# Performance work log

Measured on AMD Instinct MI355X. Metric: run time of the kernel, lower is better.

Reference implementation:

```python
import jax, jax.numpy as jnp
import numpy as np

EPS = 1e-12
B, C, H, M, E, P = 2, 20000, 64, 8, 200000, 3


def setup_inputs() -> dict:
    key = jax.random.key(0)
    ks = jax.random.split(key, 24)
    inp = {}
    inp["features"] = jax.random.normal(ks[0], (B, C, H), jnp.float32)
    inp["positions"] = jax.random.normal(ks[1], (B, C, P), jnp.float32)
    inp["edge_index"] = jax.random.randint(ks[2], (2, E), 0, C)
    inp["degree"] = jax.random.randint(ks[3], (C,), 1, 33).astype(jnp.float32)
    inp["cell_node_indices"] = jax.random.randint(ks[4], (C, M), 0, C)
    mask = (jax.random.uniform(ks[5], (C, M)) > 0.3).astype(jnp.float32)
    inp["cell_node_mask"] = mask.at[:, 0].set(1.0)  # first node always valid (pad semantics)

    def lin(k, fan_in, fan_out):
        return (jax.random.normal(k, (fan_in, fan_out), jnp.float32) / np.sqrt(fan_in)).astype(jnp.float32)

    # message MLP: Linear(2H+4 -> H), SiLU, Linear(H -> H)
    inp["W1"] = lin(ks[6], 2 * H + 4, H); inp["b1"] = jnp.zeros((H,), jnp.float32)
    inp["W2"] = lin(ks[7], H, H);         inp["b2"] = jnp.zeros((H,), jnp.float32)
    # position MLP: Linear(H -> H), SiLU, Linear(H -> 1)
    inp["P1"] = lin(ks[8], H, H);  inp["pb1"] = jnp.zeros((H,), jnp.float32)
    inp["P2"] = lin(ks[9], H, 1);  inp["pb2"] = jnp.zeros((1,), jnp.float32)
    # update MLP: Linear(2H -> H), SiLU, Linear(H -> H)
    inp["U1"] = lin(ks[10], 2 * H, H); inp["ub1"] = jnp.zeros((H,), jnp.float32)
    inp["U2"] = lin(ks[11], H, H);     inp["ub2"] = jnp.zeros((H,), jnp.float32)
    return inp


def _mlp(x, Wa, ba, Wb, bb):
    return jax.nn.silu(x @ Wa + ba) @ Wb + bb


def _forward(features, positions, edge_index, degree, cell_node_indices, cell_node_mask,
             W1, b1, W2, b2, P1, pb1, P2, pb2, U1, ub1, U2, ub2):
    src, dst = edge_index[0], edge_index[1]
    # gather padded node positions per cell: [B, C, M, P]
    node_pos = positions[:, cell_node_indices]

    h_src = features[:, src]                      # [B,E,H]
    h_dst = features[:, dst]
    rel = positions[:, src] - positions[:, dst]   # [B,E,P]
    dist = jnp.linalg.norm(rel, axis=-1, keepdims=True)  # [B,E,1]

    sp = node_pos[:, src]                         # [B,E,M,P]
    dp = node_pos[:, dst]
    mx = cell_node_mask[src]                      # [E,M]
    my = cell_node_mask[dst]

    # pairwise distances [B,E,M,M] via gram trick (avoids [B,E,M,M,P] intermediate)
    sp2 = jnp.sum(sp * sp, -1)                    # [B,E,M]
    dp2 = jnp.sum(dp * dp, -1)
    cross = jnp.einsum('bemp,benp->bemn', sp, dp)
    d = jnp.sqrt(jnp.maximum(sp2[..., :, None] + dp2[..., None, :] - 2.0 * cross, 0.0) + EPS)

    # masked pairwise-distance sum
    w = mx[:, :, None] * my[:, None, :]           # [E,M,M]
    pairwise = jnp.sum(d * w[None], axis=(-1, -2))  # [B,E]

    # centroid distance
    denx = jnp.maximum(mx.sum(-1, keepdims=True), EPS)  # [E,1]
    deny = jnp.maximum(my.sum(-1, keepdims=True), EPS)
    cx = jnp.sum(sp * mx[None, :, :, None], axis=2) / denx[None]  # [B,E,P]
    cy = jnp.sum(dp * my[None, :, :, None], axis=2) / deny[None]
    centroid = jnp.linalg.norm(cx - cy, axis=-1)  # [B,E]

    # Hausdorff distance (masked min/max)
    inf = jnp.float32(jnp.inf)
    d_xy = jnp.where(my[None, :, None, :] <= 0, inf, d)
    min_xy = jnp.where(mx[None] <= 0, 0.0, d_xy.min(-1))  # [B,E,M]
    h_xy = min_xy.max(-1)                                  # [B,E]
    d_yx = jnp.where(mx[None, :, None, :] <= 0, inf, jnp.swapaxes(d, -1, -2))
    min_yx = jnp.where(my[None] <= 0, 0.0, d_yx.min(-1))
    h_yx = min_yx.max(-1)
    haus = jnp.maximum(h_xy, h_yx)

    invariants = jnp.concatenate([dist, pairwise[..., None], centroid[..., None], haus[..., None]], -1)  # [B,E,4]
    msg_in = jnp.concatenate([h_src, h_dst, invariants], -1)  # [B,E,2H+4]
    messages = _mlp(msg_in, W1, b1, W2, b2)                   # [B,E,H]

    # scatter-aggregate into destination cells, degree-normalize
    agg = jnp.zeros_like(features).at[:, dst].add(messages)
    agg = agg / jnp.maximum(degree, 1.0)[None, :, None]

    # position update
    wts = jnp.tanh(_mlp(messages, P1, pb1, P2, pb2))          # [B,E,1]
    pos_upd = jnp.zeros_like(positions).at[:, dst].add(wts * rel)

    new_features = features + _mlp(jnp.concatenate([features, agg], -1), U1, ub1, U2, ub2)
    new_positions = positions + pos_upd
    return new_features, new_positions


def reference(features, positions, edge_index, degree, cell_node_indices, cell_node_mask,
              W1, b1, W2, b2, P1, pb1, P2, pb2, U1, ub1, U2, ub2):
    return _forward(features, positions, edge_index, degree, cell_node_indices, cell_node_mask,
                    W1, b1, W2, b2, P1, pb1, P2, pb2, U1, ub1, U2, ub2)
```

## Files before the change

### kernel.cpp

```cpp
#include <hip/hip_runtime.h>
#include <hip/hip_bf16.h>

#define B_ 2
#define C_ 20000
#define H_ 64
#define M_ 8
#define E_ 200000
#define P_ 3
#define EPS_ 1e-12f
#define ET_ (E_ / 64)

typedef __attribute__((ext_vector_type(8))) short short8;
typedef __attribute__((ext_vector_type(4))) float float4v;

__device__ __forceinline__ float silu_(float x) {
    return x / (1.f + __expf(-x));
}
__device__ __forceinline__ float tanh_fast_(float x) {
    float ex = __expf(2.f * x);
    return 1.f - 2.f / (ex + 1.f);
}
__device__ __forceinline__ unsigned short f2b(float f) {
    unsigned u = __float_as_uint(f);
    unsigned r = (u + 0x7FFF + ((u >> 16) & 1)) >> 16;
    return (unsigned short)r;
}
__device__ __forceinline__ float b2f(unsigned short h) {
    return __uint_as_float(((unsigned)h) << 16);
}
__device__ __forceinline__ unsigned pk2u(float a, float b) {
    __hip_bfloat162 h = __float22bfloat162_rn(make_float2(a, b));
    unsigned u; __builtin_memcpy(&u, &h, sizeof(u)); return u;
}

#define W1S_OFF 0
#define W2S_OFF 8192
#define P1S_OFF 12288
#define U1S_OFF 16384
#define U2S_OFF 24576
#define WBUF_ELEMS 28672

#define NB_PREP   120
#define NB_FEATB  2500
#define NB_DESC   157
#define NB_HIST   782
#define NB_COMBO  (NB_PREP + NB_FEATB + NB_DESC + NB_HIST)

#define NB_GEOM   3125
#define NB_AGGZ   2500
#define NB_PCPY   118
#define NB_GEOMK  (NB_GEOM + NB_AGGZ + NB_PCPY)

__global__ __launch_bounds__(256) void combo_kernel(
    const float* __restrict__ W1, const float* __restrict__ W2,
    const float* __restrict__ P1, const float* __restrict__ U1,
    const float* __restrict__ U2, unsigned short* __restrict__ wbuf,
    const float* __restrict__ feat, unsigned short* __restrict__ featb,
    const float* __restrict__ pos, const int* __restrict__ cni,
    const float* __restrict__ mask, float* __restrict__ desc,
    const int* __restrict__ ei, int* __restrict__ cnt)
{
    const int bid = blockIdx.x;
    if (bid < NB_PREP) {
        int t = bid * 256 + threadIdx.x;
        if (t >= WBUF_ELEMS) return;
        const float* W; int e;
        if (t < W2S_OFF)      { W = W1; e = t; }
        else if (t < U1S_OFF) { W = (t < P1S_OFF) ? W2 : P1; e = (t < P1S_OFF) ? t - W2S_OFF : t - P1S_OFF; }
        else if (t < U2S_OFF) { W = U1; e = t - U1S_OFF; }
        else                  { W = U2; e = t - U2S_OFF; }
        int j = e & 7, lane = (e >> 3) & 63, nt = (e >> 9) & 3, kk = e >> 11;
        int k = kk * 32 + ((lane >> 4) * 8) + j;
        int n = nt * 16 + (lane & 15);
        wbuf[t] = f2b(W[k * 64 + n]);
    } else if (bid < NB_PREP + NB_FEATB) {
        int t = (bid - NB_PREP) * 256 + threadIdx.x;
        float4 v = *(const float4*)&feat[(size_t)t * 4];
        *(uint2*)&featb[(size_t)t * 4] = make_uint2(pk2u(v.x, v.y), pk2u(v.z, v.w));
    } else if (bid < NB_PREP + NB_FEATB + NB_DESC) {
        int tid = (bid - NB_PREP - NB_FEATB) * 256 + threadIdx.x;
        if (tid >= B_ * C_) return;
        int b = tid / C_, c = tid - b * C_;
        const float* pb = pos + (size_t)b * C_ * P_;
        float4* D = (float4*)(desc + (size_t)tid * 40);
        int4 n0 = *(const int4*)&cni[c*8];
        int4 n1 = *(const int4*)&cni[c*8 + 4];
        float4 m0 = *(const float4*)&mask[c*8];
        float4 m1 = *(const float4*)&mask[c*8 + 4];
        int ni[8] = {n0.x, n0.y, n0.z, n0.w, n1.x, n1.y, n1.z, n1.w};
        float mm[8] = {m0.x, m0.y, m0.z, m0.w, m1.x, m1.y, m1.z, m1.w};
        float sx = 0.f, sy = 0.f, sz = 0.f, sm = 0.f;
        #pragma unroll
        for (int m = 0; m < 8; ++m) {
            float x = pb[ni[m]*3+0], y = pb[ni[m]*3+1], z = pb[ni[m]*3+2];
            D[m] = make_float4(x, y, z, mm[m]);
            sx += x * mm[m]; sy += y * mm[m]; sz += z * mm[m]; sm += mm[m];
        }
        float inv = 1.f / fmaxf(sm, EPS_);
        D[8] = make_float4(sx * inv, sy * inv, sz * inv, sm);
        D[9] = make_float4(pb[c*3+0], pb[c*3+1], pb[c*3+2], 0.f);
    } else {
        int e = (bid - NB_PREP - NB_FEATB - NB_DESC) * 256 + threadIdx.x;
        if (e >= E_) return;
        atomicAdd(&cnt[ei[E_ + e]], 1);
    }
}

__global__ __launch_bounds__(256) void alloc_kernel(
    const int* __restrict__ cnt, int* __restrict__ cursor, int* __restrict__ total)
{
    int idx = blockIdx.x * 256 + threadIdx.x;
    int lane = threadIdx.x & 63;
    int v = (idx < C_) ? cnt[idx] : 0;
    int inc = v;
    #pragma unroll
    for (int s = 1; s < 64; s <<= 1) {
        int n = __shfl_up(inc, s);
        if (lane >= s) inc += n;
    }
    int wtot = __shfl(inc, 63);
    int base = 0;
    if (lane == 0) base = atomicAdd(total, wtot);
    base = __shfl(base, 0);
    if (idx < C_) cursor[idx] = base + inc - v;
}

__global__ __launch_bounds__(256) void scatter_kernel(
    const int* __restrict__ ei, int* __restrict__ cursor,
    int2* __restrict__ sedge)
{
    int e = blockIdx.x * 256 + threadIdx.x;
    if (e >= E_) return;
    int s = ei[e], d = ei[E_ + e];
    int slot = atomicAdd(&cursor[d], 1);
    sedge[slot] = make_int2(s, d);
}

__global__ __launch_bounds__(256) void geom_kernel(
    const int2* __restrict__ sedge, const float* __restrict__ desc,
    float* __restrict__ inv8,
    float* __restrict__ aggf, const float* __restrict__ pos,
    float* __restrict__ out_pos)
{
    const int bid = blockIdx.x;
    if (bid >= NB_GEOM) {
        if (bid < NB_GEOM + NB_AGGZ) {
            int t = (bid - NB_GEOM) * 256 + threadIdx.x;
            ((float4*)aggf)[t] = make_float4(0.f, 0.f, 0.f, 0.f);
        } else {
            int t = (bid - NB_GEOM - NB_AGGZ) * 256 + threadIdx.x;
            if (t < (B_ * C_ * P_) / 4)
                ((float4*)out_pos)[t] = ((const float4*)pos)[t];
        }
        return;
    }
    int gid = bid * 256 + threadIdx.x;
    int b = gid / E_, i = gid - b * E_;
    int2 sd = sedge[i];
    const float4* Ds = (const float4*)(desc + ((size_t)b * C_ + sd.x) * 40);
    const float4* Dd = (const float4*)(desc + ((size_t)b * C_ + sd.y) * 40);
    const float INFV = __builtin_inff();
    float4 S[8];
    float a_i[8], infm_i[8], rowmin[8];
    #pragma unroll
    for (int k = 0; k < 8; ++k) {
        S[k] = Ds[k];
        a_i[k] = S[k].x*S[k].x + S[k].y*S[k].y + S[k].z*S[k].z + EPS_;
        infm_i[k] = (S[k].w > 0.f) ? 0.f : INFV;
        rowmin[k] = INFV;
    }
    float pair = 0.f, hyx = 0.f;
    #pragma unroll
    for (int j = 0; j < 8; ++j) {
        float4 Dj = Dd[j];
        float dp2 = Dj.x*Dj.x + Dj.y*Dj.y + Dj.z*Dj.z;
        float infm_j = (Dj.w > 0.f) ? 0.f : INFV;
        float colmin = INFV, psum = 0.f;
        #pragma unroll
        for (int k = 0; k < 8; ++k) {
            float cr = S[k].x*Dj.x + S[k].y*Dj.y + S[k].z*Dj.z;
            float t  = (a_i[k] + dp2) - 2.f*cr;
            float dd = sqrtf(fmaxf(t, EPS_));
            psum = fmaf(dd, S[k].w, psum);
            rowmin[k] = fminf(rowmin[k], dd + infm_j);
            colmin    = fminf(colmin,    dd + infm_i[k]);
        }
        pair = fmaf(Dj.w, psum, pair);
        hyx = fmaxf(hyx, (Dj.w > 0.f) ? colmin : 0.f);
    }
    float hxy = 0.f;
    #pragma unroll
    for (int k = 0; k < 8; ++k)
        hxy = fmaxf(hxy, (S[k].w > 0.f) ? rowmin[k] : 0.f);
    float4 Sc = Ds[8], Dc = Dd[8];
    float cdx = Sc.x - Dc.x, cdy = Sc.y - Dc.y, cdz = Sc.z - Dc.z;
    float4 Sp = Ds[9], Dp = Dd[9];
    float relx = Sp.x - Dp.x, rely = Sp.y - Dp.y, relz = Sp.z - Dp.z;
    float dist = sqrtf(relx*relx + rely*rely + relz*relz);
    float cen  = sqrtf(cdx*cdx + cdy*cdy + cdz*cdz);
    float haus = fmaxf(hxy, hyx);
    ((float4*)inv8)[(size_t)gid * 2]     = make_float4(dist, pair, cen, haus);
    ((float4*)inv8)[(size_t)gid * 2 + 1] = make_float4(relx, rely, relz, 0.f);
}

__global__ __launch_bounds__(256) void edge_kernel(
    const unsigned short* __restrict__ featb,
    const int2* __restrict__ sedge, const float* __restrict__ inv8,
    const unsigned short* __restrict__ wbuf, const float* __restrict__ W1,
    const float* __restrict__ b1, const float* __restrict__ b2,
    const float* __restrict__ pb1, const float* __restrict__ P2,
    const float* __restrict__ pb2,
    float* __restrict__ aggf, float* __restrict__ out_pos)
{
    __shared__ unsigned short lds[4 * 3328];

    const int tid  = threadIdx.x;
    const int w    = tid >> 6;
    const int lane = tid & 63;
    const int q    = lane >> 4;
    const int l16  = lane & 15;
    const int w16  = w * 16;

    const int tile = blockIdx.x;
    const int b    = tile / ET_;
    const int i0   = (tile - b * ET_) * 64;
    const int2 sd  = sedge[i0 + lane];
    const int s_l  = sd.x;
    const int d_l  = sd.y;
    const unsigned short* fb = featb + (size_t)b * C_ * H_;
    const float* ivb = inv8 + ((size_t)b * E_ + i0) * 8;

    unsigned short* Xw = lds + w * 3328;
    unsigned short* Hw = Xw + 2176;
    unsigned short* Mw = Xw;

    float4 ivhi = *(const float4*)&ivb[(w16 + l16) * 8 + 4];
    const float relx = ivhi.x, rely = ivhi.y, relz = ivhi.z;

    const int rr4 = lane >> 4, c4 = lane & 15;
    #pragma unroll
    for (int it = 0; it < 4; ++it) {
        int rloc = it * 4 + rr4;
        int r = w16 + rloc;
        int sr = __shfl(s_l, r);
        int dr = __shfl(d_l, r);
        uint2 vs = *(const uint2*)&fb[(size_t)sr * 64 + c4 * 4];
        uint2 vd = *(const uint2*)&fb[(size_t)dr * 64 + c4 * 4];
        *(uint2*)&Xw[rloc*136 + c4*4]      = vs;
        *(uint2*)&Xw[rloc*136 + 64 + c4*4] = vd;
    }

    float4v acc[4];
    #pragma unroll
    for (int nt = 0; nt < 4; ++nt) {
        float bv = b1[nt*16 + l16];
        acc[nt] = (float4v){bv, bv, bv, bv};
    }
    #pragma unroll
    for (int kk = 0; kk < 4; ++kk) {
        short8 a = *(const short8*)&Xw[l16*136 + kk*32 + q*8];
        #pragma unroll
        for (int nt = 0; nt < 4; ++nt) {
            short8 bf = *(const short8*)&wbuf[W1S_OFF + (((kk*4 + nt)*64) + lane) * 8];
            acc[nt] = __builtin_amdgcn_mfma_f32_16x16x32_bf16(a, bf, acc[nt], 0, 0, 0);
        }
    }
    float4 iv[4];
    #pragma unroll
    for (int i = 0; i < 4; ++i)
        iv[i] = *(const float4*)&ivb[(w16 + q*4 + i) * 8];
    #pragma unroll
    for (int nt = 0; nt < 4; ++nt) {
        float wa = W1[128*64 + nt*16 + l16];
        float wb = W1[129*64 + nt*16 + l16];
        float wc = W1[130*64 + nt*16 + l16];
        float wd = W1[131*64 + nt*16 + l16];
        #pragma unroll
        for (int i = 0; i < 4; ++i)
            acc[nt][i] += iv[i].x*wa + iv[i].y*wb + iv[i].z*wc + iv[i].w*wd;
    }
    #pragma unroll
    for (int nt = 0; nt < 4; ++nt)
        #pragma unroll
        for (int i = 0; i < 4; ++i)
            Hw[(q*4 + i)*72 + nt*16 + l16] = f2b(silu_(acc[nt][i]));

    float4v mac[4];
    #pragma unroll
    for (int nt = 0; nt < 4; ++nt) {
        float bv = b2[nt*16 + l16];
        mac[nt] = (float4v){bv, bv, bv, bv};
    }
    #pragma unroll
    for (int kk = 0; kk < 2; ++kk) {
        short8 a = *(const short8*)&Hw[l16*72 + kk*32 + q*8];
        #pragma unroll
        for (int nt = 0; nt < 4; ++nt) {
            short8 bf = *(const short8*)&wbuf[W2S_OFF + (((kk*4 + nt)*64) + lane) * 8];
            mac[nt] = __builtin_amdgcn_mfma_f32_16x16x32_bf16(a, bf, mac[nt], 0, 0, 0);
        }
    }
    #pragma unroll
    for (int nt = 0; nt < 4; ++nt)
        #pragma unroll
        for (int i = 0; i < 4; ++i)
            Mw[(q*4 + i)*72 + nt*16 + l16] = f2b(mac[nt][i]);

    float4v gac[4];
    #pragma unroll
    for (int nt = 0; nt < 4; ++nt) {
        float bv = pb1[nt*16 + l16];
        gac[nt] = (float4v){bv, bv, bv, bv};
    }
    #pragma unroll
    for (int kk = 0; kk < 2; ++kk) {
        short8 a = *(const short8*)&Mw[l16*72 + kk*32 + q*8];
        #pragma unroll
        for (int nt = 0; nt < 4; ++nt) {
            short8 bf = *(const short8*)&wbuf[P1S_OFF + (((kk*4 + nt)*64) + lane) * 8];
            gac[nt] = __builtin_amdgcn_mfma_f32_16x16x32_bf16(a, bf, gac[nt], 0, 0, 0);
        }
    }
    float p2v[4];
    #pragma unroll
    for (int nt = 0; nt < 4; ++nt) p2v[nt] = P2[nt*16 + l16];
    const float pb2v = pb2[0];

    #pragma unroll
    for (int i = 0; i < 4; ++i) {
        float p = 0.f;
        #pragma unroll
        for (int nt = 0; nt < 4; ++nt) p += silu_(gac[nt][i]) * p2v[nt];
        p += __shfl_xor(p, 8);
        p += __shfl_xor(p, 4);
        p += __shfl_xor(p, 2);
        p += __shfl_xor(p, 1);
        float wt = tanh_fast_(p + pb2v);
        if (l16 == 0) *(float*)&Mw[(q*4 + i)*72 + 64] = wt;
    }

    float* aggB = aggf + (size_t)b * C_ * 64;
    float* opB  = out_pos + (size_t)b * C_ * 3;

    float mrow[16];
    #pragma unroll
    for (int rr = 0; rr < 16; ++rr) mrow[rr] = b2f(Mw[rr*72 + lane]);
    float wtl = *(const float*)&Mw[l16*72 + 64];

    int dprev = __shfl(d_l, w16);
    float colacc = 0.f, pxa = 0.f, pya = 0.f, pza = 0.f;
    #pragma unroll
    for (int rr = 0; rr < 16; ++rr) {
        int dcur = __shfl(d_l, w16 + rr);
        if (dcur != dprev) {
            atomicAdd(&aggB[(size_t)dprev * 64 + lane], colacc);
            if (lane < 3) {
                float v = (lane == 0) ? pxa : (lane == 1) ? pya : pza;
                atomicAdd(&opB[(size_t)dprev * 3 + lane], v);
            }
            colacc = 0.f; pxa = 0.f; pya = 0.f; pza = 0.f;
            dprev = dcur;
        }
        float wt = __shfl(wtl, rr);
        colacc += mrow[rr];
        pxa = fmaf(wt, __shfl(relx, rr), pxa);
        pya = fmaf(wt, __shfl(rely, rr), pya);
        pza = fmaf(wt, __shfl(relz, rr), pza);
    }
    atomicAdd(&aggB[(size_t)dprev * 64 + lane], colacc);
    if (lane < 3) {
        float v = (lane == 0) ? pxa : (lane == 1) ? pya : pza;
        atomicAdd(&opB[(size_t)dprev * 3 + lane], v);
    }
}

__global__ __launch_bounds__(256) void node_kernel(
    const float* __restrict__ feat, const unsigned short* __restrict__ featb,
    const float* __restrict__ aggf, const float* __restrict__ deg,
    const unsigned short* __restrict__ wbuf,
    const float* __restrict__ ub1, const float* __restrict__ ub2,
    float* __restrict__ out_feat)
{
    __shared__ unsigned short lds[4 * 3328];

    const int tid  = threadIdx.x;
    const int w    = tid >> 6;
    const int lane = tid & 63;
    const int q    = lane >> 4;
    const int l16  = lane & 15;
    const int g0   = blockIdx.x * 64;

    unsigned short* Xw = lds + w * 3328;
    unsigned short* Hw = Xw + 2176;

    const int rr4 = lane >> 4, c4 = lane & 15;
    #pragma unroll
    for (int it = 0; it < 4; ++it) {
        int rloc = it * 4 + rr4;
        int g = g0 + w*16 + rloc;
        int gc = (g >= C_) ? g - C_ : g;
        float sc = 1.f / fmaxf(deg[gc], 1.f);
        uint2  vf = *(const uint2*)&featb[(size_t)g * 64 + c4 * 4];
        float4 va = *(const float4*)&aggf[(size_t)g * 64 + c4 * 4];
        *(uint2*)&Xw[rloc*136 + c4*4]      = vf;
        *(uint2*)&Xw[rloc*136 + 64 + c4*4] =
            make_uint2(pk2u(va.x*sc, va.y*sc), pk2u(va.z*sc, va.w*sc));
    }

    float4v acc[4];
    #pragma unroll
    for (int nt = 0; nt < 4; ++nt) {
        float bv = ub1[nt*16 + l16];
        acc[nt] = (float4v){bv, bv, bv, bv};
    }
    #pragma unroll
    for (int kk = 0; kk < 4; ++kk) {
        short8 a = *(const short8*)&Xw[l16*136 + kk*32 + q*8];
        #pragma unroll
        for (int nt = 0; nt < 4; ++nt) {
            short8 bf = *(const short8*)&wbuf[U1S_OFF + (((kk*4 + nt)*64) + lane) * 8];
            acc[nt] = __builtin_amdgcn_mfma_f32_16x16x32_bf16(a, bf, acc[nt], 0, 0, 0);
        }
    }
    #pragma unroll
    for (int nt = 0; nt < 4; ++nt)
        #pragma unroll
        for (int i = 0; i < 4; ++i)
            Hw[(q*4 + i)*72 + nt*16 + l16] = f2b(silu_(acc[nt][i]));

    float4v oac[4];
    #pragma unroll
    for (int nt = 0; nt < 4; ++nt) {
        float bv = ub2[nt*16 + l16];
        oac[nt] = (float4v){bv, bv, bv, bv};
    }
    #pragma unroll
    for (int kk = 0; kk < 2; ++kk) {
        short8 a = *(const short8*)&Hw[l16*72 + kk*32 + q*8];
        #pragma unroll
        for (int nt = 0; nt < 4; ++nt) {
            short8 bf = *(const short8*)&wbuf[U2S_OFF + (((kk*4 + nt)*64) + lane) * 8];
            oac[nt] = __builtin_amdgcn_mfma_f32_16x16x32_bf16(a, bf, oac[nt], 0, 0, 0);
        }
    }
    #pragma unroll
    for (int nt = 0; nt < 4; ++nt)
        #pragma unroll
        for (int i = 0; i < 4; ++i) {
            size_t idx = (size_t)(g0 + w*16 + q*4 + i) * 64 + nt*16 + l16;
            out_feat[idx] = feat[idx] + oac[nt][i];
        }
}

extern "C" void kernel_launch(void* const* d_in, const int* in_sizes, int n_in,
                              void* d_out, int out_size, void* d_ws, size_t ws_size,
                              hipStream_t stream) {
    const float* feat = (const float*)d_in[0];
    const float* pos  = (const float*)d_in[1];
    const int*   ei   = (const int*)d_in[2];
    const float* deg  = (const float*)d_in[3];
    const int*   cni  = (const int*)d_in[4];
    const float* mask = (const float*)d_in[5];
    const float* W1   = (const float*)d_in[6];
    const float* b1   = (const float*)d_in[7];
    const float* W2   = (const float*)d_in[8];
    const float* b2   = (const float*)d_in[9];
    const float* P1   = (const float*)d_in[10];
    const float* pb1  = (const float*)d_in[11];
    const float* P2   = (const float*)d_in[12];
    const float* pb2  = (const float*)d_in[13];
    const float* U1   = (const float*)d_in[14];
    const float* ub1  = (const float*)d_in[15];
    const float* U2   = (const float*)d_in[16];
    const float* ub2  = (const float*)d_in[17];

    float* out_feat = (float*)d_out;
    float* out_pos  = out_feat + (size_t)B_ * C_ * H_;

    float* desc = (float*)d_ws;
    float* aggf = desc + (size_t)B_ * C_ * 40;
    unsigned short* featb = (unsigned short*)(aggf + (size_t)B_ * C_ * 64);
    unsigned short* wbuf  = featb + (size_t)B_ * C_ * 64;
    int* cnt    = (int*)(wbuf + WBUF_ELEMS);
    int* total  = cnt + C_;
    int* cursor = total + 4;
    int2* sedge = (int2*)(cursor + C_);
    float* inv8 = (float*)(sedge + E_);

    hipMemsetAsync(cnt, 0, (C_ + 4) * sizeof(int), stream);

    combo_kernel<<<NB_COMBO, 256, 0, stream>>>(
        W1, W2, P1, U1, U2, wbuf, feat, featb, pos, cni, mask, desc, ei, cnt);

    alloc_kernel<<<(C_ + 255) / 256, 256, 0, stream>>>(cnt, cursor, total);
    scatter_kernel<<<(E_ + 255) / 256, 256, 0, stream>>>(ei, cursor, sedge);

    geom_kernel<<<NB_GEOMK, 256, 0, stream>>>(sedge, desc, inv8, aggf, pos, out_pos);

    edge_kernel<<<B_ * ET_, 256, 0, stream>>>(
        featb, sedge, inv8, wbuf, W1, b1, b2, pb1, P2, pb2, aggf, out_pos);

    node_kernel<<<(B_ * C_) / 64, 256, 0, stream>>>(
        feat, featb, aggf, deg, wbuf, ub1, ub2, out_feat);
}
```

Baseline: 247.3 us.

## Store cell descriptors in bf16 and split each edge's geometry across four lanes

Cell descriptors (node positions, mask, centroid, own position) are now packed as bf16 instead of fp32, halving the bytes gathered per edge. The geometry kernel assigns four lanes per edge, each handling two destination nodes, and combines partial Hausdorff and pairwise results with cross-lane shuffles. The block count doubles to match. Source descriptors are loaded redundantly by all four lanes, and bf16 positions reduce the precision of the distance invariants.

```diff
diff --git a/kernel.cpp b/kernel.cpp
--- a/kernel.cpp
+++ b/kernel.cpp
@@ -32,6 +32,13 @@
     __hip_bfloat162 h = __float22bfloat162_rn(make_float2(a, b));
     unsigned u; __builtin_memcpy(&u, &h, sizeof(u)); return u;
 }
+__device__ __forceinline__ float4 up4_(const unsigned short* p) {
+    uint2 u = *(const uint2*)p;
+    return make_float4(__uint_as_float(u.x << 16),
+                       __uint_as_float(u.x & 0xffff0000u),
+                       __uint_as_float(u.y << 16),
+                       __uint_as_float(u.y & 0xffff0000u));
+}
 
 #define W1S_OFF 0
 #define W2S_OFF 8192
@@ -46,7 +53,7 @@
 #define NB_HIST   782
 #define NB_COMBO  (NB_PREP + NB_FEATB + NB_DESC + NB_HIST)
 
-#define NB_GEOM   3125
+#define NB_GEOM   6250
 #define NB_AGGZ   2500
 #define NB_PCPY   118
 #define NB_GEOMK  (NB_GEOM + NB_AGGZ + NB_PCPY)
@@ -57,7 +64,7 @@
     const float* __restrict__ U2, unsigned short* __restrict__ wbuf,
     const float* __restrict__ feat, unsigned short* __restrict__ featb,
     const float* __restrict__ pos, const int* __restrict__ cni,
-    const float* __restrict__ mask, float* __restrict__ desc,
+    const float* __restrict__ mask, unsigned short* __restrict__ descb,
     const int* __restrict__ ei, int* __restrict__ cnt)
 {
     const int bid = blockIdx.x;
@@ -82,7 +89,7 @@
         if (tid >= B_ * C_) return;
         int b = tid / C_, c = tid - b * C_;
         const float* pb = pos + (size_t)b * C_ * P_;
-        float4* D = (float4*)(desc + (size_t)tid * 40);
+        unsigned short* R = descb + (size_t)tid * 40;
         int4 n0 = *(const int4*)&cni[c*8];
         int4 n1 = *(const int4*)&cni[c*8 + 4];
         float4 m0 = *(const float4*)&mask[c*8];
@@ -93,12 +100,12 @@
         #pragma unroll
         for (int m = 0; m < 8; ++m) {
             float x = pb[ni[m]*3+0], y = pb[ni[m]*3+1], z = pb[ni[m]*3+2];
-            D[m] = make_float4(x, y, z, mm[m]);
+            *(uint2*)&R[m*4] = make_uint2(pk2u(x, y), pk2u(z, mm[m]));
             sx += x * mm[m]; sy += y * mm[m]; sz += z * mm[m]; sm += mm[m];
         }
         float inv = 1.f / fmaxf(sm, EPS_);
-        D[8] = make_float4(sx * inv, sy * inv, sz * inv, sm);
-        D[9] = make_float4(pb[c*3+0], pb[c*3+1], pb[c*3+2], 0.f);
+        *(uint2*)&R[32] = make_uint2(pk2u(sx*inv, sy*inv), pk2u(sz*inv, sm));
+        *(uint2*)&R[36] = make_uint2(pk2u(pb[c*3+0], pb[c*3+1]), pk2u(pb[c*3+2], 0.f));
     } else {
         int e = (bid - NB_PREP - NB_FEATB - NB_DESC) * 256 + threadIdx.x;
         if (e >= E_) return;
@@ -137,7 +144,7 @@
 }
 
 __global__ __launch_bounds__(256) void geom_kernel(
-    const int2* __restrict__ sedge, const float* __restrict__ desc,
+    const int2* __restrict__ sedge, const unsigned short* __restrict__ descb,
     float* __restrict__ inv8,
     float* __restrict__ aggf, const float* __restrict__ pos,
     float* __restrict__ out_pos)
@@ -154,25 +161,33 @@
         }
         return;
     }
-    int gid = bid * 256 + threadIdx.x;
-    int b = gid / E_, i = gid - b * E_;
-    int2 sd = sedge[i];
-    const float4* Ds = (const float4*)(desc + ((size_t)b * C_ + sd.x) * 40);
-    const float4* Dd = (const float4*)(desc + ((size_t)b * C_ + sd.y) * 40);
+    const int tid  = threadIdx.x;
+    const int w    = tid >> 6;
+    const int lane = tid & 63;
+    const int q    = lane >> 4;
+    const int l16  = lane & 15;
+
+    const int ge = bid * 64 + w * 16 + l16;
+    const int b  = ge / E_;
+    const int i  = ge - b * E_;
+    const int2 sd = sedge[i];
+    const unsigned short* Sb = descb + ((size_t)b * C_ + sd.x) * 40;
+    const unsigned short* Db = descb + ((size_t)b * C_ + sd.y) * 40;
+
     const float INFV = __builtin_inff();
     float4 S[8];
     float a_i[8], infm_i[8], rowmin[8];
     #pragma unroll
     for (int k = 0; k < 8; ++k) {
-        S[k] = Ds[k];
+        S[k] = up4_(&Sb[k*4]);
         a_i[k] = S[k].x*S[k].x + S[k].y*S[k].y + S[k].z*S[k].z + EPS_;
         infm_i[k] = (S[k].w > 0.f) ? 0.f : INFV;
         rowmin[k] = INFV;
     }
     float pair = 0.f, hyx = 0.f;
     #pragma unroll
-    for (int j = 0; j < 8; ++j) {
-        float4 Dj = Dd[j];
+    for (int jj = 0; jj < 2; ++jj) {
+        float4 Dj = up4_(&Db[(q*2 + jj)*4]);
         float dp2 = Dj.x*Dj.x + Dj.y*Dj.y + Dj.z*Dj.z;
         float infm_j = (Dj.w > 0.f) ? 0.f : INFV;
         float colmin = INFV, psum = 0.f;
@@ -188,19 +203,29 @@
         pair = fmaf(Dj.w, psum, pair);
         hyx = fmaxf(hyx, (Dj.w > 0.f) ? colmin : 0.f);
     }
+    pair += __shfl_xor(pair, 16);  pair += __shfl_xor(pair, 32);
+    hyx = fmaxf(hyx, __shfl_xor(hyx, 16));  hyx = fmaxf(hyx, __shfl_xor(hyx, 32));
+    #pragma unroll
+    for (int k = 0; k < 8; ++k) {
+        rowmin[k] = fminf(rowmin[k], __shfl_xor(rowmin[k], 16));
+        rowmin[k] = fminf(rowmin[k], __shfl_xor(rowmin[k], 32));
+    }
     float hxy = 0.f;
     #pragma unroll
     for (int k = 0; k < 8; ++k)
         hxy = fmaxf(hxy, (S[k].w > 0.f) ? rowmin[k] : 0.f);
-    float4 Sc = Ds[8], Dc = Dd[8];
+
+    float4 Sc = up4_(&Sb[32]), Dc = up4_(&Db[32]);
     float cdx = Sc.x - Dc.x, cdy = Sc.y - Dc.y, cdz = Sc.z - Dc.z;
-    float4 Sp = Ds[9], Dp = Dd[9];
+    float4 Sp = up4_(&Sb[36]), Dp = up4_(&Db[36]);
     float relx = Sp.x - Dp.x, rely = Sp.y - Dp.y, relz = Sp.z - Dp.z;
     float dist = sqrtf(relx*relx + rely*rely + relz*relz);
     float cen  = sqrtf(cdx*cdx + cdy*cdy + cdz*cdz);
     float haus = fmaxf(hxy, hyx);
-    ((float4*)inv8)[(size_t)gid * 2]     = make_float4(dist, pair, cen, haus);
-    ((float4*)inv8)[(size_t)gid * 2 + 1] = make_float4(relx, rely, relz, 0.f);
+
+    size_t off = ((size_t)b * E_ + i) * 8;
+    if (q == 0)      *(float4*)&inv8[off]     = make_float4(dist, pair, cen, haus);
+    else if (q == 1) *(float4*)&inv8[off + 4] = make_float4(relx, rely, relz, 0.f);
 }
 
 __global__ __launch_bounds__(256) void edge_kernel(
@@ -477,10 +502,10 @@
     float* out_feat = (float*)d_out;
     float* out_pos  = out_feat + (size_t)B_ * C_ * H_;
 
-    float* desc = (float*)d_ws;
-    float* aggf = desc + (size_t)B_ * C_ * 40;
+    float* aggf = (float*)d_ws;
     unsigned short* featb = (unsigned short*)(aggf + (size_t)B_ * C_ * 64);
-    unsigned short* wbuf  = featb + (size_t)B_ * C_ * 64;
+    unsigned short* descb = featb + (size_t)B_ * C_ * 64;
+    unsigned short* wbuf  = descb + (size_t)B_ * C_ * 40;
     int* cnt    = (int*)(wbuf + WBUF_ELEMS);
     int* total  = cnt + C_;
     int* cursor = total + 4;
@@ -490,12 +515,12 @@
     hipMemsetAsync(cnt, 0, (C_ + 4) * sizeof(int), stream);
 
     combo_kernel<<<NB_COMBO, 256, 0, stream>>>(
-        W1, W2, P1, U1, U2, wbuf, feat, featb, pos, cni, mask, desc, ei, cnt);
+        W1, W2, P1, U1, U2, wbuf, feat, featb, pos, cni, mask, descb, ei, cnt);
 
     alloc_kernel<<<(C_ + 255) / 256, 256, 0, stream>>>(cnt, cursor, total);
     scatter_kernel<<<(E_ + 255) / 256, 256, 0, stream>>>(ei, cursor, sedge);
 
-    geom_kernel<<<NB_GEOMK, 256, 0, stream>>>(sedge, desc, inv8, aggf, pos, out_pos);
+    geom_kernel<<<NB_GEOMK, 256, 0, stream>>>(sedge, descb, inv8, aggf, pos, out_pos);
 
     edge_kernel<<<B_ * ET_, 256, 0, stream>>>(
         featb, sedge, inv8, wbuf, W1, b1, b2, pb1, P2, pb2, aggf, out_pos);
```

Result: faster. 232.9 us (-5.8%).
